# Kernel tuning notes

Measured on AMD Instinct MI355X. Metric: run time of the kernel, lower is better.

## Reference

```python
import jax, jax.numpy as jnp
import numpy as np

CONF_THRES = 0.25
IOU_THRES = 0.45
MAX_WH = 7680.0   # class-separation offset (class-aware NMS trick)
K = 1024          # max candidates entering NMS per image
MAX_DET = 300     # max detections returned per image


def _pairwise_iou(boxes):
    # boxes: [K,4] xyxy -> iou: [K,K]
    x1, y1, x2, y2 = boxes[:, 0], boxes[:, 1], boxes[:, 2], boxes[:, 3]
    area = (x2 - x1) * (y2 - y1)
    ix1 = jnp.maximum(x1[:, None], x1[None, :])
    iy1 = jnp.maximum(y1[:, None], y1[None, :])
    ix2 = jnp.minimum(x2[:, None], x2[None, :])
    iy2 = jnp.minimum(y2[:, None], y2[None, :])
    inter = jnp.clip(ix2 - ix1, 0.0) * jnp.clip(iy2 - iy1, 0.0)
    union = area[:, None] + area[None, :] - inter
    return inter / (union + 1e-9)


def _nms_single(pred):
    # pred: [N, 5+nc]
    xywh = pred[:, :4]
    obj = pred[:, 4]
    cls_conf = obj[:, None] * pred[:, 5:]            # [N, nc]
    score = cls_conf.max(axis=-1)                    # best-class confidence
    cls_id = cls_conf.argmax(axis=-1)                # best class

    # confidence filter (masked, fixed shape): invalid -> score sentinel -1
    masked = jnp.where(score > CONF_THRES, score, -1.0)
    top_s, top_i = jax.lax.top_k(masked, K)          # sorted descending
    keep0 = top_s > CONF_THRES                       # valid candidates

    b = xywh[top_i]                                  # [K,4]
    sc = score[top_i]
    c = cls_id[top_i].astype(pred.dtype)

    # xywh -> xyxy
    cx, cy, w, h = b[:, 0], b[:, 1], b[:, 2], b[:, 3]
    boxes = jnp.stack([cx - w / 2, cy - h / 2, cx + w / 2, cy + h / 2], axis=-1)

    # class-aware NMS: offset boxes by class index so classes never overlap
    off_boxes = boxes + (c * MAX_WH)[:, None]
    iou = _pairwise_iou(off_boxes)                   # [K,K]

    idx = jnp.arange(K)
    def body(i, keep):
        # if box i is kept, suppress all later boxes with IoU > thresh
        sup = (iou[i] > IOU_THRES) & keep[i] & (idx > i)
        return keep & ~sup
    keep = jax.lax.fori_loop(0, K, body, keep0)

    # select top MAX_DET kept detections (scores already descending)
    order = jnp.argsort(-jnp.where(keep, top_s, -1.0))[:MAX_DET]
    det = jnp.concatenate([boxes, sc[:, None], c[:, None]], axis=-1)  # [K,6]
    out = jnp.where(keep[order][:, None], det[order], 0.0)            # [MAX_DET,6]
    return out


def setup_inputs() -> dict:
    key = jax.random.key(0)
    x = jax.random.uniform(key, (16, 25200, 85), dtype=jnp.float32)
    return {"x": x}


def reference(x):
    # x: [B, N, 5+nc] raw predictions (sigmoid-activated)
    # returns [B, MAX_DET, 6] = (x1, y1, x2, y2, conf, cls), zero-padded
    return jax.vmap(_nms_single)(x)
```

## Files before the change

kernel.cpp:

```cpp
#include <hip/hip_runtime.h>
#include <hip/hip_bf16.h>
#include <stdint.h>


#define NB 16
#define NA 25200
#define NK 1024
#define ND 300
#define CAP 2048
#define NBIN 4096

__device__ __forceinline__ uint32_t fkey(float f) {
    uint32_t b = __float_as_uint(f);
    return (b & 0x80000000u) ? ~b : (b | 0x80000000u);
}

__device__ __forceinline__ int score_bin(float s) {
    float f = (s - 0.25f) * (4096.0f / 0.75f);
    int b = (int)f;
    return b > (NBIN - 1) ? (NBIN - 1) : (b < 0 ? 0 : b);
}

__global__ void score_kernel(const float* __restrict__ x,
                             float* __restrict__ scores,
                             int* __restrict__ clsid,
                             float4* __restrict__ boxes) {
    int b = blockIdx.y;
    int a = blockIdx.x * 16 + (threadIdx.x >> 4);
    int lane = threadIdx.x & 15;
    const float* p = x + (size_t)(b * NA + a) * 85;
    float obj = p[4];
    float best = -1e30f;
    int bi = 0;
#pragma unroll
    for (int r = 0; r < 5; ++r) {
        int j = lane + 16 * r;
        float v = obj * p[5 + j];
        if (v > best) { best = v; bi = j; }
    }
    for (int off = 8; off >= 1; off >>= 1) {
        float ov = __shfl_xor(best, off, 16);
        int   oi = __shfl_xor(bi,   off, 16);
        if (ov > best || (ov == best && oi < bi)) { best = ov; bi = oi; }
    }
    if (lane == 0) {
        bool q = best > 0.25f;
        scores[b * NA + a] = q ? best : -1.0f;
        clsid[b * NA + a] = bi;
        float cx = p[0], cy = p[1], w = p[2], h = p[3];
        boxes[b * NA + a] = make_float4(cx - w * 0.5f, cy - h * 0.5f,
                                        cx + w * 0.5f, cy + h * 0.5f);
    }
}

__global__ void __launch_bounds__(1024)
select_sort_kernel(const float* __restrict__ scores,
                   const float4* __restrict__ boxes,
                   const int* __restrict__ clsid,
                   float4* __restrict__ obox,
                   float* __restrict__ det,
                   unsigned long long* __restrict__ keep0w) {
    int b = blockIdx.x;
    int t = threadIdx.x;
    int wid = t >> 6, lane = t & 63;
    __shared__ unsigned int lhist[NBIN];
    __shared__ unsigned long long sk[CAP];
    __shared__ unsigned int wsum[16];
    __shared__ int sB;
    __shared__ unsigned int scnt;

    ((uint4*)lhist)[t] = make_uint4(0u, 0u, 0u, 0u);
    sk[t] = 0ULL; sk[t + 1024] = 0ULL;
    if (t == 0) { sB = -1; scnt = 0u; }
    __syncthreads();
    const float* sc = scores + b * NA;
    const float4* sc4 = (const float4*)sc;
    for (int i = t; i < NA / 4; i += 1024) {
        float4 s4 = sc4[i];
        if (s4.x > 0.25f) atomicAdd(&lhist[score_bin(s4.x)], 1u);
        if (s4.y > 0.25f) atomicAdd(&lhist[score_bin(s4.y)], 1u);
        if (s4.z > 0.25f) atomicAdd(&lhist[score_bin(s4.z)], 1u);
        if (s4.w > 0.25f) atomicAdd(&lhist[score_bin(s4.w)], 1u);
    }
    __syncthreads();

    uint4 hv = ((const uint4*)lhist)[t];
    unsigned int mysum = hv.x + hv.y + hv.z + hv.w;
    unsigned int ssfx = mysum;
#pragma unroll
    for (int off = 1; off < 64; off <<= 1) {
        unsigned int v = __shfl_down(ssfx, off);
        if (lane + off < 64) ssfx += v;
    }
    if (lane == 0) wsum[wid] = ssfx;
    __syncthreads();
    unsigned int tail = 0;
    for (int w2 = wid + 1; w2 < 16; ++w2) tail += wsum[w2];
    unsigned int S_t = ssfx + tail;
    unsigned int Snext = S_t - mysum;
    unsigned int s3 = hv.w + Snext;
    unsigned int s2 = hv.z + s3;
    unsigned int s1 = hv.y + s2;
    unsigned int s0 = hv.x + s1;
    int loc = -1;
    if (s3 >= NK) loc = t * 4 + 3;
    else if (s2 >= NK) loc = t * 4 + 2;
    else if (s1 >= NK) loc = t * 4 + 1;
    else if (s0 >= NK) loc = t * 4 + 0;
#pragma unroll
    for (int off = 32; off >= 1; off >>= 1) {
        int o = __shfl_xor(loc, off);
        loc = o > loc ? o : loc;
    }
    if ((t & 63) == 0) atomicMax(&sB, loc);
    __syncthreads();
    int B = sB < 0 ? 0 : sB;

    for (int i = t; i < NA / 4; i += 1024) {
        float4 s4 = sc4[i];
        float se[4] = {s4.x, s4.y, s4.z, s4.w};
#pragma unroll
        for (int e = 0; e < 4; ++e) {
            float s = se[e];
            int a = i * 4 + e;
            bool q = (s > 0.25f) && (score_bin(s) >= B);
            unsigned long long m = __ballot(q);
            if (q) {
                int nbelow = __popcll(m & ((1ULL << lane) - 1));
                int leader = __ffsll((long long)m) - 1;
                unsigned int base = 0;
                if (lane == leader)
                    base = atomicAdd(&scnt, (unsigned int)__popcll(m));
                base = __shfl(base, leader);
                unsigned int pos = base + nbelow;
                if (pos < CAP)
                    sk[pos] =
                        ((unsigned long long)fkey(s) << 32) | (uint32_t)(~a);
            }
        }
    }
    __syncthreads();

    const int e1 = t, e2 = t + 1024;
    unsigned long long v1 = sk[e1];
    unsigned long long v2 = sk[e2];
    __syncthreads();
    for (int k = 2; k <= CAP; k <<= 1) {
        for (int j = k >> 1; j > 0; j >>= 1) {
            if (j >= 1024) {
                unsigned long long lo = v1 < v2 ? v1 : v2;
                unsigned long long hi = v1 < v2 ? v2 : v1;
                v1 = hi; v2 = lo;
            } else if (j >= 64) {
                sk[e1] = v1; sk[e2] = v2;
                __syncthreads();
                unsigned long long p1 = sk[e1 ^ j], p2 = sk[e2 ^ j];
                __syncthreads();
                {
                    bool takeMax = (((e1 & j) == 0) == ((e1 & k) == 0));
                    bool g = p1 > v1;
                    v1 = (takeMax == g) ? p1 : v1;
                }
                {
                    bool takeMax = (((e2 & j) == 0) == ((e2 & k) == 0));
                    bool g = p2 > v2;
                    v2 = (takeMax == g) ? p2 : v2;
                }
            } else {
                {
                    unsigned long long p1 =
                        (unsigned long long)__shfl_xor((long long)v1, j);
                    bool takeMax = (((e1 & j) == 0) == ((e1 & k) == 0));
                    bool g = p1 > v1;
                    v1 = (takeMax == g) ? p1 : v1;
                }
                {
                    unsigned long long p2 =
                        (unsigned long long)__shfl_xor((long long)v2, j);
                    bool takeMax = (((e2 & j) == 0) == ((e2 & k) == 0));
                    bool g = p2 > v2;
                    v2 = (takeMax == g) ? p2 : v2;
                }
            }
        }
    }
    unsigned long long key = v1;
    uint32_t u = (uint32_t)(key >> 32);
    int a = (u == 0) ? 0 : (int)(~(uint32_t)key);
    uint32_t fb = (u & 0x80000000u) ? (u ^ 0x80000000u) : ~u;
    float s = __uint_as_float(fb);
    float4 bx = boxes[b * NA + a];
    float c = (float)clsid[b * NA + a];
    float off = c * 7680.0f;
    obox[b * NK + t] =
        make_float4(bx.x + off, bx.y + off, bx.z + off, bx.w + off);
    float* dr = det + (size_t)(b * NK + t) * 8;
    dr[0] = bx.x; dr[1] = bx.y; dr[2] = bx.z; dr[3] = bx.w;
    dr[4] = s; dr[5] = c;
    bool keep0 = s > 0.25f;
    unsigned long long bal = __ballot(keep0);
    if ((t & 63) == 0) keep0w[b * 16 + (t >> 6)] = bal;
}

__global__ void mask_kernel(const float4* __restrict__ obox,
                            unsigned long long* __restrict__ maskm) {
    int cb = blockIdx.x, rb = blockIdx.y, b = blockIdx.z;
    if (cb > rb) return;
    int t = threadIdx.x;
    int i = rb * 64 + t;
    __shared__ float4 cbox[64];
    __shared__ float carea[64];
    int j0 = cb * 64;
    float4 c4 = obox[b * NK + j0 + t];
    cbox[t] = c4;
    carea[t] = (c4.z - c4.x) * (c4.w - c4.y);
    __syncthreads();
    float4 r4 = obox[b * NK + i];
    float ra = (r4.z - r4.x) * (r4.w - r4.y);
    unsigned long long word = 0;
    for (int jj = 0; jj < 64; ++jj) {
        int j = j0 + jj;
        float4 o = cbox[jj];
        if (j < i && fabsf(r4.x - o.x) < 3840.0f) {
            float ix1 = fmaxf(r4.x, o.x), iy1 = fmaxf(r4.y, o.y);
            float ix2 = fminf(r4.z, o.z), iy2 = fminf(r4.w, o.w);
            float iw = fmaxf(ix2 - ix1, 0.0f), ih = fmaxf(iy2 - iy1, 0.0f);
            float inter = iw * ih;
            float uni = ra + carea[jj] - inter;
            float iou = inter / (uni + 1e-9f);
            if (iou > 0.45f) word |= (1ULL << jj);
        }
    }
    maskm[(size_t)(b * 16 + cb) * NK + i] = word;
}

__global__ void __launch_bounds__(1024)
jacobi_out_kernel(const unsigned long long* __restrict__ maskm,
                  const unsigned long long* __restrict__ keep0w,
                  const float* __restrict__ det,
                  float* __restrict__ out) {
    int b = blockIdx.x;
    int t = threadIdx.x;
    int wid = t >> 6, lane = t & 63;
    __shared__ unsigned long long aliveS[16];
    __shared__ int changedS;
    __shared__ int list[ND];
    __shared__ int totalS;

    unsigned long long row[16];
#pragma unroll
    for (int w = 0; w < 16; ++w)
        row[w] = (w <= wid) ? maskm[(size_t)(b * 16 + w) * NK + t] : 0ULL;
    bool keep0 = (keep0w[b * 16 + wid] >> lane) & 1ULL;
    if (t < 16) aliveS[t] = keep0w[b * 16 + t];
    __syncthreads();

    for (int it = 0; it < NK; ++it) {
        if (t == 0) changedS = 0;
        unsigned long long aw[16];
#pragma unroll
        for (int w = 0; w < 16; ++w) aw[w] = aliveS[w];
        __syncthreads();
        unsigned long long sup = 0;
#pragma unroll
        for (int w = 0; w < 16; ++w) sup |= aw[w] & row[w];
        bool newalive = keep0 && (sup == 0);
        unsigned long long bal = __ballot(newalive);
        if (lane == 0) {
            if (bal != aw[wid]) { atomicOr(&changedS, 1); aliveS[wid] = bal; }
        }
        __syncthreads();
        if (!changedS) break;
    }

    if (t < 64) {
        unsigned long long av = (lane < 16) ? aliveS[lane] : 0ULL;
        int cnt = (lane < 16) ? __popcll(av) : 0;
        int pre = cnt;
        for (int off = 1; off < 64; off <<= 1) {
            int v = __shfl_up(pre, off);
            if (lane >= off) pre += v;
        }
        int total = __shfl(pre, 63);
        int base = pre - cnt;
        if (lane == 0) totalS = total;
        if (lane < 16) {
            unsigned long long m = av;
            int pos = base;
            while (m && pos < ND) {
                int bit = __ffsll((long long)m) - 1;
                list[pos++] = lane * 64 + bit;
                m &= m - 1;
            }
        }
    }
    __syncthreads();
    if (t < ND) {
        float vals[6] = {0, 0, 0, 0, 0, 0};
        if (t < totalS) {
            const float* dr = det + (size_t)(b * NK + list[t]) * 8;
#pragma unroll
            for (int c = 0; c < 6; ++c) vals[c] = dr[c];
        }
        float* o = out + (size_t)(b * ND + t) * 6;
#pragma unroll
        for (int c = 0; c < 6; ++c) o[c] = vals[c];
    }
}

extern "C" void kernel_launch(void* const* d_in, const int* in_sizes, int n_in,
                              void* d_out, int out_size, void* d_ws, size_t ws_size,
                              hipStream_t stream) {
    const float* x = (const float*)d_in[0];
    float* out = (float*)d_out;

    char* ws = (char*)d_ws;
    size_t off = 0;
    auto alloc = [&](size_t bytes) {
        void* p = ws + off;
        off += (bytes + 255) & ~(size_t)255;
        return p;
    };
    float* scores = (float*)alloc((size_t)NB * NA * sizeof(float));
    int* clsid = (int*)alloc((size_t)NB * NA * sizeof(int));
    float4* boxes = (float4*)alloc((size_t)NB * NA * sizeof(float4));
    float4* obox = (float4*)alloc((size_t)NB * NK * sizeof(float4));
    float* det = (float*)alloc((size_t)NB * NK * 8 * sizeof(float));
    unsigned long long* keep0w =
        (unsigned long long*)alloc((size_t)NB * 16 * sizeof(unsigned long long));
    unsigned long long* maskm =
        (unsigned long long*)alloc((size_t)NB * NK * 16 * sizeof(unsigned long long));
    (void)ws_size;

    score_kernel<<<dim3(NA / 16, NB), 256, 0, stream>>>(x, scores, clsid,
                                                        boxes);
    select_sort_kernel<<<NB, 1024, 0, stream>>>(scores, boxes, clsid, obox,
                                                det, keep0w);
    mask_kernel<<<dim3(16, 16, NB), 64, 0, stream>>>(obox, maskm);
    jacobi_out_kernel<<<NB, 1024, 0, stream>>>(maskm, keep0w, det, out);
}
```

Baseline: 83.89 us.

## Fuse select, IoU mask and suppression into one kernel with per-class sparse IoU

Merges the select/sort, mask and Jacobi suppression kernels into one block-per-image kernel that keeps boxes, scores and masks in shared memory. IoU is now computed only against earlier candidates of the same class, found through a per-class bitmask built with shared atomics, instead of a dense 64x64 tile scan. This removes two launches and the global round-trips for obox, det and the mask matrix. In exchange, the IoU work for each image runs inside a single 1024-thread block, and per-lane loops over class bits can diverge within a wavefront.

```diff
diff --git a/kernel.cpp b/kernel.cpp
--- a/kernel.cpp
+++ b/kernel.cpp
@@ -9,6 +9,7 @@
 #define ND 300
 #define CAP 2048
 #define NBIN 4096
+#define NCLS 80
 
 __device__ __forceinline__ uint32_t fkey(float f) {
     uint32_t b = __float_as_uint(f);
@@ -54,23 +55,34 @@
 }
 
 __global__ void __launch_bounds__(1024)
-select_sort_kernel(const float* __restrict__ scores,
-                   const float4* __restrict__ boxes,
-                   const int* __restrict__ clsid,
-                   float4* __restrict__ obox,
-                   float* __restrict__ det,
-                   unsigned long long* __restrict__ keep0w) {
+fused_nms_kernel(const float* __restrict__ scores,
+                 const float4* __restrict__ boxes,
+                 const int* __restrict__ clsid,
+                 float* __restrict__ out) {
     int b = blockIdx.x;
     int t = threadIdx.x;
     int wid = t >> 6, lane = t & 63;
-    __shared__ unsigned int lhist[NBIN];
-    __shared__ unsigned long long sk[CAP];
+
+    __shared__ __align__(16) char smemA[CAP * 8];
+    __shared__ __align__(16) char smemB[NBIN * 4];
+    __shared__ float2 dscl[NK];
+    __shared__ unsigned long long cmaskS[NCLS * 16];
+    __shared__ unsigned long long aliveS[16];
     __shared__ unsigned int wsum[16];
+    __shared__ int list[ND];
     __shared__ int sB;
     __shared__ unsigned int scnt;
+    __shared__ int changedS;
+    __shared__ int totalS;
+    unsigned long long* sk = (unsigned long long*)smemA;
+    float4* oboxS = (float4*)smemA;
+    unsigned int* lhist = (unsigned int*)smemB;
+    float4* dboxS = (float4*)smemB;
 
     ((uint4*)lhist)[t] = make_uint4(0u, 0u, 0u, 0u);
     sk[t] = 0ULL; sk[t + 1024] = 0ULL;
+    cmaskS[t] = 0ULL;
+    if (t < NCLS * 16 - 1024) cmaskS[1024 + t] = 0ULL;
     if (t == 0) { sB = -1; scnt = 0u; }
     __syncthreads();
     const float* sc = scores + b * NA;
@@ -184,75 +196,52 @@
             }
         }
     }
+
     unsigned long long key = v1;
     uint32_t u = (uint32_t)(key >> 32);
     int a = (u == 0) ? 0 : (int)(~(uint32_t)key);
     uint32_t fb = (u & 0x80000000u) ? (u ^ 0x80000000u) : ~u;
     float s = __uint_as_float(fb);
     float4 bx = boxes[b * NA + a];
-    float c = (float)clsid[b * NA + a];
+    int ci = clsid[b * NA + a];
+    float c = (float)ci;
     float off = c * 7680.0f;
-    obox[b * NK + t] =
-        make_float4(bx.x + off, bx.y + off, bx.z + off, bx.w + off);
-    float* dr = det + (size_t)(b * NK + t) * 8;
-    dr[0] = bx.x; dr[1] = bx.y; dr[2] = bx.z; dr[3] = bx.w;
-    dr[4] = s; dr[5] = c;
+    float4 ob = make_float4(bx.x + off, bx.y + off, bx.z + off, bx.w + off);
     bool keep0 = s > 0.25f;
     unsigned long long bal = __ballot(keep0);
-    if ((t & 63) == 0) keep0w[b * 16 + (t >> 6)] = bal;
-}
-
-__global__ void mask_kernel(const float4* __restrict__ obox,
-                            unsigned long long* __restrict__ maskm) {
-    int cb = blockIdx.x, rb = blockIdx.y, b = blockIdx.z;
-    if (cb > rb) return;
-    int t = threadIdx.x;
-    int i = rb * 64 + t;
-    __shared__ float4 cbox[64];
-    __shared__ float carea[64];
-    int j0 = cb * 64;
-    float4 c4 = obox[b * NK + j0 + t];
-    cbox[t] = c4;
-    carea[t] = (c4.z - c4.x) * (c4.w - c4.y);
-    __syncthreads();
-    float4 r4 = obox[b * NK + i];
+    if (lane == 0) aliveS[wid] = bal;
+    __syncthreads();
+    oboxS[t] = ob;
+    dboxS[t] = bx;
+    dscl[t] = make_float2(s, c);
+    atomicOr(&cmaskS[ci * 16 + wid], 1ULL << lane);
+    __syncthreads();
+
+    unsigned long long row[16];
+#pragma unroll
+    for (int w = 0; w < 16; ++w) row[w] = 0ULL;
+    float4 r4 = ob;
     float ra = (r4.z - r4.x) * (r4.w - r4.y);
-    unsigned long long word = 0;
-    for (int jj = 0; jj < 64; ++jj) {
-        int j = j0 + jj;
-        float4 o = cbox[jj];
-        if (j < i && fabsf(r4.x - o.x) < 3840.0f) {
+    for (int w = 0; w <= wid; ++w) {
+        unsigned long long bits = cmaskS[ci * 16 + w];
+        if (w == wid)
+            bits &= (lane == 0) ? 0ULL : ((1ULL << lane) - 1ULL);
+        unsigned long long rbits = 0ULL;
+        while (bits) {
+            int bit = __ffsll((long long)bits) - 1;
+            bits &= bits - 1;
+            float4 o = oboxS[w * 64 + bit];
+            float carea = (o.z - o.x) * (o.w - o.y);
             float ix1 = fmaxf(r4.x, o.x), iy1 = fmaxf(r4.y, o.y);
             float ix2 = fminf(r4.z, o.z), iy2 = fminf(r4.w, o.w);
             float iw = fmaxf(ix2 - ix1, 0.0f), ih = fmaxf(iy2 - iy1, 0.0f);
             float inter = iw * ih;
-            float uni = ra + carea[jj] - inter;
+            float uni = ra + carea - inter;
             float iou = inter / (uni + 1e-9f);
-            if (iou > 0.45f) word |= (1ULL << jj);
-        }
-    }
-    maskm[(size_t)(b * 16 + cb) * NK + i] = word;
-}
-
-__global__ void __launch_bounds__(1024)
-jacobi_out_kernel(const unsigned long long* __restrict__ maskm,
-                  const unsigned long long* __restrict__ keep0w,
-                  const float* __restrict__ det,
-                  float* __restrict__ out) {
-    int b = blockIdx.x;
-    int t = threadIdx.x;
-    int wid = t >> 6, lane = t & 63;
-    __shared__ unsigned long long aliveS[16];
-    __shared__ int changedS;
-    __shared__ int list[ND];
-    __shared__ int totalS;
-
-    unsigned long long row[16];
-#pragma unroll
-    for (int w = 0; w < 16; ++w)
-        row[w] = (w <= wid) ? maskm[(size_t)(b * 16 + w) * NK + t] : 0ULL;
-    bool keep0 = (keep0w[b * 16 + wid] >> lane) & 1ULL;
-    if (t < 16) aliveS[t] = keep0w[b * 16 + t];
+            if (iou > 0.45f) rbits |= (1ULL << bit);
+        }
+        row[w] = rbits;
+    }
     __syncthreads();
 
     for (int it = 0; it < NK; ++it) {
@@ -265,9 +254,9 @@
 #pragma unroll
         for (int w = 0; w < 16; ++w) sup |= aw[w] & row[w];
         bool newalive = keep0 && (sup == 0);
-        unsigned long long bal = __ballot(newalive);
+        unsigned long long nb = __ballot(newalive);
         if (lane == 0) {
-            if (bal != aw[wid]) { atomicOr(&changedS, 1); aliveS[wid] = bal; }
+            if (nb != aw[wid]) { atomicOr(&changedS, 1); aliveS[wid] = nb; }
         }
         __syncthreads();
         if (!changedS) break;
@@ -277,9 +266,9 @@
         unsigned long long av = (lane < 16) ? aliveS[lane] : 0ULL;
         int cnt = (lane < 16) ? __popcll(av) : 0;
         int pre = cnt;
-        for (int off = 1; off < 64; off <<= 1) {
-            int v = __shfl_up(pre, off);
-            if (lane >= off) pre += v;
+        for (int off2 = 1; off2 < 64; off2 <<= 1) {
+            int v = __shfl_up(pre, off2);
+            if (lane >= off2) pre += v;
         }
         int total = __shfl(pre, 63);
         int base = pre - cnt;
@@ -298,13 +287,15 @@
     if (t < ND) {
         float vals[6] = {0, 0, 0, 0, 0, 0};
         if (t < totalS) {
-            const float* dr = det + (size_t)(b * NK + list[t]) * 8;
-#pragma unroll
-            for (int c = 0; c < 6; ++c) vals[c] = dr[c];
+            int i = list[t];
+            float4 db = dboxS[i];
+            float2 sl = dscl[i];
+            vals[0] = db.x; vals[1] = db.y; vals[2] = db.z; vals[3] = db.w;
+            vals[4] = sl.x; vals[5] = sl.y;
         }
         float* o = out + (size_t)(b * ND + t) * 6;
 #pragma unroll
-        for (int c = 0; c < 6; ++c) o[c] = vals[c];
+        for (int c2 = 0; c2 < 6; ++c2) o[c2] = vals[c2];
     }
 }
 
@@ -324,18 +315,9 @@
     float* scores = (float*)alloc((size_t)NB * NA * sizeof(float));
     int* clsid = (int*)alloc((size_t)NB * NA * sizeof(int));
     float4* boxes = (float4*)alloc((size_t)NB * NA * sizeof(float4));
-    float4* obox = (float4*)alloc((size_t)NB * NK * sizeof(float4));
-    float* det = (float*)alloc((size_t)NB * NK * 8 * sizeof(float));
-    unsigned long long* keep0w =
-        (unsigned long long*)alloc((size_t)NB * 16 * sizeof(unsigned long long));
-    unsigned long long* maskm =
-        (unsigned long long*)alloc((size_t)NB * NK * 16 * sizeof(unsigned long long));
     (void)ws_size;
 
     score_kernel<<<dim3(NA / 16, NB), 256, 0, stream>>>(x, scores, clsid,
                                                         boxes);
-    select_sort_kernel<<<NB, 1024, 0, stream>>>(scores, boxes, clsid, obox,
-                                                det, keep0w);
-    mask_kernel<<<dim3(16, 16, NB), 64, 0, stream>>>(obox, maskm);
-    jacobi_out_kernel<<<NB, 1024, 0, stream>>>(maskm, keep0w, det, out);
-}
+    fused_nms_kernel<<<NB, 1024, 0, stream>>>(scores, boxes, clsid, out);
+}
```

New measurement: 90.88 us. 8.3% more time.
